# Kernel optimization log

Measured on AMD Instinct MI355X. Metric: run time of the kernel, lower is better.

Reference implementation:

```python
import jax, jax.numpy as jnp
import numpy as np

N_NODES = 100000
N_EDGES = 3200000
F_IN = 16


def gcn_conv(x, edge_index, W, b):
    """PyG GCNConv: x' = D^{-1/2} (A + I) D^{-1/2} (x W) + b,
    with degree computed after adding self-loops."""
    n = x.shape[0]
    xw = x @ W  # [N, F_out]
    row, col = edge_index[0], edge_index[1]  # messages flow row -> col
    ones = jnp.ones(row.shape, dtype=x.dtype)
    deg = jax.ops.segment_sum(ones, col, num_segments=n) + 1.0  # +1 for self-loop
    dinv = jax.lax.rsqrt(deg)  # [N]
    norm = dinv[row] * dinv[col]  # [E]
    msg = xw[row] * norm[:, None]  # [E, F_out]
    out = jax.ops.segment_sum(msg, col, num_segments=n)
    out = out + xw * (1.0 / deg)[:, None]  # self-loop term: norm = 1/deg
    return out + b


def setup_inputs() -> dict:
    key = jax.random.key(0)
    ks = jax.random.split(key, 8)
    x = jax.random.normal(ks[0], (N_NODES, F_IN), dtype=jnp.float32)
    edge_index = jax.random.randint(ks[1], (2, N_EDGES), 0, N_NODES, dtype=jnp.int32)
    # GCNConv weights (glorot in PyG; random normal scaled for the reference)
    W1 = jax.random.normal(ks[2], (F_IN, 4), dtype=jnp.float32) * 0.3
    W2 = jax.random.normal(ks[3], (4, 2), dtype=jnp.float32) * 0.5
    W3 = jax.random.normal(ks[4], (2, 1), dtype=jnp.float32) * 0.7
    b1 = jnp.zeros((4,), jnp.float32)
    b2 = jnp.zeros((2,), jnp.float32)
    b3 = jnp.zeros((1,), jnp.float32)
    return {"x": x, "edge_index": edge_index, "W1": W1, "b1": b1,
            "W2": W2, "b2": b2, "W3": W3, "b3": b3}


def reference(x, edge_index, W1, b1, W2, b2, W3, b3):
    # encode(): GCNConv -> relu -> GCNConv -> relu -> GCNConv -> tanh
    # (dropout is identity in eval mode)
    h = jax.nn.relu(gcn_conv(x, edge_index, W1, b1))
    h = jax.nn.relu(gcn_conv(h, edge_index, W2, b2))
    return jnp.tanh(gcn_conv(h, edge_index, W3, b3))  # [N, 1]
```

## Files before the change

kernel.cpp:

```cpp
#include <hip/hip_runtime.h>
#include <math.h>


static constexpr int BLK    = 256;
static constexpr int BSHIFT = 7;
static constexpr int BCOLS  = 128;
static constexpr int NBMAX  = 1024;
static constexpr int CAP    = 5120;
static constexpr int PAD    = 16;
static constexpr int PBLK   = 512;
static constexpr int PITER  = 13;
static constexpr int PCHUNK = PBLK * PITER;
static constexpr int SBLK   = 512;
static constexpr int GBLK   = 512;

__global__ void zero_cnt_kernel(int* __restrict__ cnt, int len) {
    int i = blockIdx.x * blockDim.x + threadIdx.x;
    if (i < len) cnt[i] = 0;
}

__global__ __launch_bounds__(PBLK) void partition_kernel(
        const int* __restrict__ row, const int* __restrict__ col,
        int* __restrict__ cnt, unsigned int* __restrict__ part,
        int e, int nbuck) {
    __shared__ unsigned int   staged[PCHUNK];
    __shared__ unsigned short bkid[PCHUNK];
    __shared__ int hist[NBMAX];
    __shared__ int excl[NBMAX];
    __shared__ int gbase[NBMAX];
    __shared__ int sh[PBLK];
    const int t = (int)threadIdx.x;
    for (int j = t; j < NBMAX; j += PBLK) hist[j] = 0;
    __syncthreads();

    const int blockstart = blockIdx.x * PCHUNK;
    const int m = min(PCHUNK, e - blockstart);

    unsigned int pay[PITER];
    int bks[PITER], rnk[PITER];
#pragma unroll
    for (int i = 0; i < PITER; ++i) {
        int idx = blockstart + i * PBLK + t;
        if (idx < e) {
            int c = col[idx], r = row[idx];
            bks[i] = c >> BSHIFT;
            pay[i] = ((unsigned int)(c & (BCOLS - 1)) << 17) | (unsigned int)r;
            rnk[i] = atomicAdd(&hist[bks[i]], 1);
        } else {
            bks[i] = -1;
        }
    }
    __syncthreads();

    int a0 = hist[2 * t], a1 = hist[2 * t + 1];
    sh[t] = a0 + a1;
    __syncthreads();
    for (int off = 1; off < PBLK; off <<= 1) {
        int v = (t >= off) ? sh[t - off] : 0;
        __syncthreads();
        sh[t] += v;
        __syncthreads();
    }
    int pairExcl = sh[t] - (a0 + a1);
    excl[2 * t]     = pairExcl;
    excl[2 * t + 1] = pairExcl + a0;
    for (int j = t; j < nbuck; j += PBLK) {
        int h = hist[j];
        gbase[j] = h ? atomicAdd(&cnt[j * PAD], h) : 0;
    }
    __syncthreads();

#pragma unroll
    for (int i = 0; i < PITER; ++i) {
        if (bks[i] >= 0) {
            int pos = excl[bks[i]] + rnk[i];
            staged[pos] = pay[i];
            bkid[pos]   = (unsigned short)bks[i];
        }
    }
    __syncthreads();

    for (int k = t; k < m; k += PBLK) {
        int bk  = bkid[k];
        int off2 = gbase[bk] + (k - excl[bk]);
        if (off2 < CAP)
            part[(size_t)bk * CAP + off2] = staged[k];
    }
}

__global__ __launch_bounds__(SBLK) void sort_y1_kernel(
        unsigned int* __restrict__ part, const int* __restrict__ cnt,
        const float* __restrict__ x, const float* __restrict__ W1,
        int* __restrict__ rs, int* __restrict__ re, float* __restrict__ dinv,
        float* __restrict__ y1, int n) {
    __shared__ unsigned int   staged[CAP];
    __shared__ unsigned int   sorted[CAP];
    __shared__ unsigned short srank[CAP];
    __shared__ int hist[BCOLS];
    __shared__ int scanb[BCOLS];
    const int b = blockIdx.x;
    const int m = min(cnt[b * PAD], CAP);
    const size_t segbase = (size_t)b * CAP;

    if (threadIdx.x < BCOLS) hist[threadIdx.x] = 0;
    __syncthreads();
    for (int k = threadIdx.x; k < m; k += SBLK) {
        unsigned int v = part[segbase + k];
        staged[k] = v;
        srank[k] = (unsigned short)atomicAdd(&hist[v >> 17], 1);
    }
    __syncthreads();

    if (threadIdx.x < BCOLS) scanb[threadIdx.x] = hist[threadIdx.x];
    __syncthreads();
    for (int off = 1; off < BCOLS; off <<= 1) {
        int v = 0;
        if (threadIdx.x < BCOLS && (int)threadIdx.x >= off)
            v = scanb[threadIdx.x - off];
        __syncthreads();
        if (threadIdx.x < BCOLS) scanb[threadIdx.x] += v;
        __syncthreads();
    }

    for (int k = threadIdx.x; k < m; k += SBLK) {
        unsigned int v = staged[k];
        int lc = (int)(v >> 17);
        sorted[(scanb[lc] - hist[lc]) + (int)srank[k]] = v & 0x1FFFFu;
    }
    __syncthreads();

    for (int k = threadIdx.x; k < m; k += SBLK)
        part[segbase + k] = sorted[k];

    int lc = (int)threadIdx.x >> 2;
    int f  = (int)threadIdx.x & 3;
    int node = b * BCOLS + lc;
    if (node < n) {
        int deg = hist[lc];
        float di = rsqrtf((float)(deg + 1));
        if (f == 0) {
            int start = (int)segbase + (scanb[lc] - deg);
            rs[node] = start;
            re[node] = start + deg;
            dinv[node] = di;
        }
        const float4* x4 = (const float4*)x + (size_t)node * 4;
        float4 r0 = x4[0], r1 = x4[1], r2 = x4[2], r3 = x4[3];
        float a = 0.0f;
        a = fmaf(r0.x, W1[0 * 4 + f], a);  a = fmaf(r0.y, W1[1 * 4 + f], a);
        a = fmaf(r0.z, W1[2 * 4 + f], a);  a = fmaf(r0.w, W1[3 * 4 + f], a);
        a = fmaf(r1.x, W1[4 * 4 + f], a);  a = fmaf(r1.y, W1[5 * 4 + f], a);
        a = fmaf(r1.z, W1[6 * 4 + f], a);  a = fmaf(r1.w, W1[7 * 4 + f], a);
        a = fmaf(r2.x, W1[8 * 4 + f], a);  a = fmaf(r2.y, W1[9 * 4 + f], a);
        a = fmaf(r2.z, W1[10 * 4 + f], a); a = fmaf(r2.w, W1[11 * 4 + f], a);
        a = fmaf(r3.x, W1[12 * 4 + f], a); a = fmaf(r3.y, W1[13 * 4 + f], a);
        a = fmaf(r3.z, W1[14 * 4 + f], a); a = fmaf(r3.w, W1[15 * 4 + f], a);
        y1[node * 4 + f] = a * di;
    }
}

template <int F, int FN, int ACT, int SUBW>
__global__ __launch_bounds__(GBLK) void gather_kernel(
        const int* __restrict__ rs, const int* __restrict__ re,
        const unsigned int* __restrict__ csr,
        const float* __restrict__ y, const float* __restrict__ dinv,
        const float* __restrict__ bias, const float* __restrict__ Wn,
        float* __restrict__ outv, int n) {
    int t = blockIdx.x * GBLK + (int)threadIdx.x;
    int node = t / SUBW;
    int lane = t % SUBW;
    if (node >= n) return;
    int s = rs[node], tend = re[node];
    float acc[F];
#pragma unroll
    for (int f = 0; f < F; ++f) acc[f] = 0.0f;
    const float4* y4 = (const float4*)y;
    const float2* y2p = (const float2*)y;
    for (int k = s + lane; k < tend; k += SUBW) {
        int r = (int)csr[k];
        if constexpr (F == 4) {
            float4 a = y4[r];
            acc[0] += a.x; acc[1] += a.y; acc[2] += a.z; acc[3] += a.w;
        } else if constexpr (F == 2) {
            float2 a = y2p[r];
            acc[0] += a.x; acc[1] += a.y;
        } else {
            acc[0] += y[r];
        }
    }
#pragma unroll
    for (int off = SUBW / 2; off > 0; off >>= 1)
#pragma unroll
        for (int f = 0; f < F; ++f) acc[f] += __shfl_xor(acc[f], off);
    if (lane == 0) {
        float di = dinv[node];
        float h[F];
#pragma unroll
        for (int f = 0; f < F; ++f) {
            float z = di * (acc[f] + y[node * F + f]) + bias[f];
            if (ACT == 1) z = fmaxf(z, 0.0f);
            if (ACT == 2) z = tanhf(z);
            h[f] = z;
        }
        if constexpr (FN > 0) {
            float o[FN];
#pragma unroll
            for (int g = 0; g < FN; ++g) o[g] = 0.0f;
#pragma unroll
            for (int f = 0; f < F; ++f)
#pragma unroll
                for (int g = 0; g < FN; ++g)
                    o[g] = fmaf(h[f], Wn[f * FN + g], o[g]);
#pragma unroll
            for (int g = 0; g < FN; ++g) outv[node * FN + g] = o[g] * di;
        } else {
#pragma unroll
            for (int f = 0; f < F; ++f) outv[node * F + f] = h[f];
        }
    }
}

extern "C" void kernel_launch(void* const* d_in, const int* in_sizes, int n_in,
                              void* d_out, int out_size, void* d_ws, size_t ws_size,
                              hipStream_t stream) {
    const float* x  = (const float*)d_in[0];
    const int*   ei = (const int*)d_in[1];
    const float* W1 = (const float*)d_in[2];
    const float* b1 = (const float*)d_in[3];
    const float* W2 = (const float*)d_in[4];
    const float* b2 = (const float*)d_in[5];
    const float* W3 = (const float*)d_in[6];
    const float* b3 = (const float*)d_in[7];
    float* out = (float*)d_out;

    const int n = in_sizes[0] / 16;
    const int e = in_sizes[1] / 2;
    const int* row = ei;
    const int* col = ei + e;

    const int nbuck = (n + BCOLS - 1) / BCOLS;

    size_t off = 0;
    auto take = [&](size_t cnt_) {
        char* p = (char*)d_ws + off * 4;
        off += (cnt_ + 15) & ~(size_t)15;
        return p;
    };
    int* cnt           = (int*)take((size_t)nbuck * PAD);
    unsigned int* part = (unsigned int*)take((size_t)nbuck * CAP);
    int* rs            = (int*)take(n);
    int* re            = (int*)take(n);
    float* dinv        = (float*)take(n);
    float* y1          = (float*)take(4 * n);
    float* y2          = (float*)take(2 * n);
    float* y3          = (float*)take(n);

    zero_cnt_kernel<<<(nbuck * PAD + BLK - 1) / BLK, BLK, 0, stream>>>(cnt, nbuck * PAD);

    const int pnb = (e + PCHUNK - 1) / PCHUNK;
    partition_kernel<<<pnb, PBLK, 0, stream>>>(row, col, cnt, part, e, nbuck);

    sort_y1_kernel<<<nbuck, SBLK, 0, stream>>>(part, cnt, x, W1, rs, re, dinv, y1, n);

    constexpr int SUBW = 8;
    const int gg = (n * SUBW + GBLK - 1) / GBLK;

    gather_kernel<4, 2, 1, SUBW><<<gg, GBLK, 0, stream>>>(rs, re, part, y1, dinv, b1, W2, y2, n);
    gather_kernel<2, 1, 1, SUBW><<<gg, GBLK, 0, stream>>>(rs, re, part, y2, dinv, b2, W3, y3, n);
    gather_kernel<1, 0, 2, SUBW><<<gg, GBLK, 0, stream>>>(rs, re, part, y3, dinv, b3, nullptr, out, n);
}
```

Baseline: 113.3 us.

## Fuse all GCN stages into one cooperative persistent kernel with grid syncs

Replaces the six separate launches (zero, partition, sort, three gathers) with a single cooperative kernel that uses grid-wide syncs between phases. Each phase loops over its work with a persistent grid sized from occupancy. The aim is to remove kernel launch gaps and tail idling between dependent stages. In exchange it adds grid.sync costs, reduces parallelism in the partition phase (larger chunks, 1024-thread blocks), and the persistent grid may under-occupy the gather phases.

```diff
diff --git a/kernel.cpp b/kernel.cpp
--- a/kernel.cpp
+++ b/kernel.cpp
@@ -1,223 +1,237 @@
 #include <hip/hip_runtime.h>
+#include <hip/hip_cooperative_groups.h>
 #include <math.h>
 
-
-static constexpr int BLK    = 256;
+namespace cg = cooperative_groups;
+
+
 static constexpr int BSHIFT = 7;
 static constexpr int BCOLS  = 128;
 static constexpr int NBMAX  = 1024;
 static constexpr int CAP    = 5120;
 static constexpr int PAD    = 16;
-static constexpr int PBLK   = 512;
-static constexpr int PITER  = 13;
-static constexpr int PCHUNK = PBLK * PITER;
-static constexpr int SBLK   = 512;
-static constexpr int GBLK   = 512;
-
-__global__ void zero_cnt_kernel(int* __restrict__ cnt, int len) {
-    int i = blockIdx.x * blockDim.x + threadIdx.x;
-    if (i < len) cnt[i] = 0;
-}
-
-__global__ __launch_bounds__(PBLK) void partition_kernel(
-        const int* __restrict__ row, const int* __restrict__ col,
-        int* __restrict__ cnt, unsigned int* __restrict__ part,
-        int e, int nbuck) {
-    __shared__ unsigned int   staged[PCHUNK];
-    __shared__ unsigned short bkid[PCHUNK];
-    __shared__ int hist[NBMAX];
-    __shared__ int excl[NBMAX];
-    __shared__ int gbase[NBMAX];
-    __shared__ int sh[PBLK];
-    const int t = (int)threadIdx.x;
-    for (int j = t; j < NBMAX; j += PBLK) hist[j] = 0;
-    __syncthreads();
-
-    const int blockstart = blockIdx.x * PCHUNK;
-    const int m = min(PCHUNK, e - blockstart);
-
-    unsigned int pay[PITER];
-    int bks[PITER], rnk[PITER];
-#pragma unroll
-    for (int i = 0; i < PITER; ++i) {
-        int idx = blockstart + i * PBLK + t;
-        if (idx < e) {
-            int c = col[idx], r = row[idx];
-            bks[i] = c >> BSHIFT;
-            pay[i] = ((unsigned int)(c & (BCOLS - 1)) << 17) | (unsigned int)r;
-            rnk[i] = atomicAdd(&hist[bks[i]], 1);
-        } else {
-            bks[i] = -1;
-        }
-    }
-    __syncthreads();
-
-    int a0 = hist[2 * t], a1 = hist[2 * t + 1];
-    sh[t] = a0 + a1;
-    __syncthreads();
-    for (int off = 1; off < PBLK; off <<= 1) {
-        int v = (t >= off) ? sh[t - off] : 0;
-        __syncthreads();
-        sh[t] += v;
-        __syncthreads();
-    }
-    int pairExcl = sh[t] - (a0 + a1);
-    excl[2 * t]     = pairExcl;
-    excl[2 * t + 1] = pairExcl + a0;
-    for (int j = t; j < nbuck; j += PBLK) {
-        int h = hist[j];
-        gbase[j] = h ? atomicAdd(&cnt[j * PAD], h) : 0;
-    }
-    __syncthreads();
-
-#pragma unroll
-    for (int i = 0; i < PITER; ++i) {
-        if (bks[i] >= 0) {
-            int pos = excl[bks[i]] + rnk[i];
-            staged[pos] = pay[i];
-            bkid[pos]   = (unsigned short)bks[i];
-        }
-    }
-    __syncthreads();
-
-    for (int k = t; k < m; k += PBLK) {
-        int bk  = bkid[k];
-        int off2 = gbase[bk] + (k - excl[bk]);
-        if (off2 < CAP)
-            part[(size_t)bk * CAP + off2] = staged[k];
+static constexpr int TB     = 1024;
+static constexpr int PITER  = 7;
+static constexpr int PCHUNK = TB * PITER;
+static constexpr int SUBW   = 8;
+
+static constexpr int SMEM_BYTES = 55296;
+
+struct Params {
+    const float* x;
+    const int* row;
+    const int* col;
+    const float* W1; const float* b1;
+    const float* W2; const float* b2;
+    const float* W3; const float* b3;
+    int* cnt;
+    unsigned int* part;
+    int* rs; int* re;
+    float* dinv;
+    float* y1; float* y2; float* y3;
+    float* out;
+    int n, e, nbuck, nchunk;
+};
+
+template <int F, int FN, int ACT>
+__device__ __forceinline__ void gather_layer(
+        const Params& p, const float* __restrict__ y,
+        const float* __restrict__ bias, const float* __restrict__ Wn,
+        float* __restrict__ outv, int gsize) {
+    const int total = p.n * SUBW;
+    for (int tt = blockIdx.x * TB + (int)threadIdx.x; tt < total; tt += gsize * TB) {
+        int node = tt >> 3;
+        int lane = tt & 7;
+        int s = p.rs[node], tend = p.re[node];
+        float acc[F];
+#pragma unroll
+        for (int f = 0; f < F; ++f) acc[f] = 0.0f;
+        for (int k = s + lane; k < tend; k += SUBW) {
+            int r = (int)p.part[k];
+            if constexpr (F == 4) {
+                float4 a = ((const float4*)y)[r];
+                acc[0] += a.x; acc[1] += a.y; acc[2] += a.z; acc[3] += a.w;
+            } else if constexpr (F == 2) {
+                float2 a = ((const float2*)y)[r];
+                acc[0] += a.x; acc[1] += a.y;
+            } else {
+                acc[0] += y[r];
+            }
+        }
+#pragma unroll
+        for (int off = SUBW / 2; off > 0; off >>= 1)
+#pragma unroll
+            for (int f = 0; f < F; ++f) acc[f] += __shfl_xor(acc[f], off);
+        if (lane == 0) {
+            float di = p.dinv[node];
+            float h[F];
+#pragma unroll
+            for (int f = 0; f < F; ++f) {
+                float z = di * (acc[f] + y[node * F + f]) + bias[f];
+                if (ACT == 1) z = fmaxf(z, 0.0f);
+                if (ACT == 2) z = tanhf(z);
+                h[f] = z;
+            }
+            if constexpr (FN > 0) {
+                float o[FN];
+#pragma unroll
+                for (int g = 0; g < FN; ++g) o[g] = 0.0f;
+#pragma unroll
+                for (int f = 0; f < F; ++f)
+#pragma unroll
+                    for (int g = 0; g < FN; ++g)
+                        o[g] = fmaf(h[f], Wn[f * FN + g], o[g]);
+#pragma unroll
+                for (int g = 0; g < FN; ++g) outv[node * FN + g] = o[g] * di;
+            } else {
+#pragma unroll
+                for (int f = 0; f < F; ++f) outv[node * F + f] = h[f];
+            }
+        }
     }
 }
 
-__global__ __launch_bounds__(SBLK) void sort_y1_kernel(
-        unsigned int* __restrict__ part, const int* __restrict__ cnt,
-        const float* __restrict__ x, const float* __restrict__ W1,
-        int* __restrict__ rs, int* __restrict__ re, float* __restrict__ dinv,
-        float* __restrict__ y1, int n) {
-    __shared__ unsigned int   staged[CAP];
-    __shared__ unsigned int   sorted[CAP];
-    __shared__ unsigned short srank[CAP];
-    __shared__ int hist[BCOLS];
-    __shared__ int scanb[BCOLS];
-    const int b = blockIdx.x;
-    const int m = min(cnt[b * PAD], CAP);
-    const size_t segbase = (size_t)b * CAP;
-
-    if (threadIdx.x < BCOLS) hist[threadIdx.x] = 0;
-    __syncthreads();
-    for (int k = threadIdx.x; k < m; k += SBLK) {
-        unsigned int v = part[segbase + k];
-        staged[k] = v;
-        srank[k] = (unsigned short)atomicAdd(&hist[v >> 17], 1);
+__global__ __launch_bounds__(TB, 8) void gcn_mega_kernel(Params p) {
+    cg::grid_group grid = cg::this_grid();
+    __shared__ __align__(16) unsigned char smem[SMEM_BYTES];
+    const int t = (int)threadIdx.x;
+    const int gsize = (int)gridDim.x;
+
+    for (int i = blockIdx.x * TB + t; i < p.nbuck * PAD; i += gsize * TB)
+        p.cnt[i] = 0;
+    grid.sync();
+
+    {
+        unsigned int*   staged = (unsigned int*)(smem);
+        unsigned short* bkid   = (unsigned short*)(smem + 28672);
+        int* hist  = (int*)(smem + 43008);
+        int* excl  = (int*)(smem + 47104);
+        int* gbase = (int*)(smem + 51200);
+        for (int chunk = blockIdx.x; chunk < p.nchunk; chunk += gsize) {
+            hist[t] = 0;
+            __syncthreads();
+            const int bs = chunk * PCHUNK;
+            const int m = min(PCHUNK, p.e - bs);
+            unsigned int pay[PITER];
+            int bks[PITER], rnk[PITER];
+#pragma unroll
+            for (int i = 0; i < PITER; ++i) {
+                int idx = bs + i * TB + t;
+                if (idx < p.e) {
+                    int c = p.col[idx], r = p.row[idx];
+                    bks[i] = c >> BSHIFT;
+                    pay[i] = ((unsigned int)(c & (BCOLS - 1)) << 17) | (unsigned int)r;
+                    rnk[i] = atomicAdd(&hist[bks[i]], 1);
+                } else {
+                    bks[i] = -1;
+                }
+            }
+            __syncthreads();
+            int h = hist[t];
+            excl[t] = h;
+            __syncthreads();
+            for (int off = 1; off < NBMAX; off <<= 1) {
+                int v = (t >= off) ? excl[t - off] : 0;
+                __syncthreads();
+                excl[t] += v;
+                __syncthreads();
+            }
+            int ex = excl[t] - h;
+            int gb = (h > 0) ? atomicAdd(&p.cnt[t * PAD], h) : 0;
+            excl[t]  = ex;
+            gbase[t] = gb;
+            __syncthreads();
+#pragma unroll
+            for (int i = 0; i < PITER; ++i) {
+                if (bks[i] >= 0) {
+                    int pos = excl[bks[i]] + rnk[i];
+                    staged[pos] = pay[i];
+                    bkid[pos]   = (unsigned short)bks[i];
+                }
+            }
+            __syncthreads();
+            for (int k = t; k < m; k += TB) {
+                int bk = bkid[k];
+                int o2 = gbase[bk] + (k - excl[bk]);
+                if (o2 < CAP)
+                    p.part[(size_t)bk * CAP + o2] = staged[k];
+            }
+            __syncthreads();
+        }
     }
-    __syncthreads();
-
-    if (threadIdx.x < BCOLS) scanb[threadIdx.x] = hist[threadIdx.x];
-    __syncthreads();
-    for (int off = 1; off < BCOLS; off <<= 1) {
-        int v = 0;
-        if (threadIdx.x < BCOLS && (int)threadIdx.x >= off)
-            v = scanb[threadIdx.x - off];
-        __syncthreads();
-        if (threadIdx.x < BCOLS) scanb[threadIdx.x] += v;
-        __syncthreads();
+    grid.sync();
+
+    {
+        unsigned int*   staged = (unsigned int*)(smem);
+        unsigned int*   sorted = (unsigned int*)(smem + 20480);
+        unsigned short* srank  = (unsigned short*)(smem + 40960);
+        int* hist  = (int*)(smem + 51200);
+        int* scanb = (int*)(smem + 51712);
+        for (int b = blockIdx.x; b < p.nbuck; b += gsize) {
+            const int m = min(p.cnt[b * PAD], CAP);
+            const size_t segbase = (size_t)b * CAP;
+            if (t < BCOLS) hist[t] = 0;
+            __syncthreads();
+            for (int k = t; k < m; k += TB) {
+                unsigned int v = p.part[segbase + k];
+                staged[k] = v;
+                srank[k] = (unsigned short)atomicAdd(&hist[v >> 17], 1);
+            }
+            __syncthreads();
+            if (t < BCOLS) scanb[t] = hist[t];
+            __syncthreads();
+            for (int off = 1; off < BCOLS; off <<= 1) {
+                int v = 0;
+                if (t < BCOLS && t >= off) v = scanb[t - off];
+                __syncthreads();
+                if (t < BCOLS) scanb[t] += v;
+                __syncthreads();
+            }
+            for (int k = t; k < m; k += TB) {
+                unsigned int v = staged[k];
+                int lc = (int)(v >> 17);
+                sorted[(scanb[lc] - hist[lc]) + (int)srank[k]] = v & 0x1FFFFu;
+            }
+            __syncthreads();
+            for (int k = t; k < m; k += TB)
+                p.part[segbase + k] = sorted[k];
+            int lc = t >> 3, sub = t & 7;
+            int node = b * BCOLS + lc;
+            if (node < p.n) {
+                int deg = hist[lc];
+                float di = rsqrtf((float)(deg + 1));
+                if (sub == 0) {
+                    int start = (int)segbase + (scanb[lc] - deg);
+                    p.rs[node] = start;
+                    p.re[node] = start + deg;
+                    p.dinv[node] = di;
+                }
+                if (sub < 4) {
+                    const float4* x4 = (const float4*)p.x + (size_t)node * 4;
+                    float4 r0 = x4[0], r1 = x4[1], r2 = x4[2], r3 = x4[3];
+                    const float* W1 = p.W1;
+                    float a = 0.0f;
+                    a = fmaf(r0.x, W1[0 * 4 + sub], a);  a = fmaf(r0.y, W1[1 * 4 + sub], a);
+                    a = fmaf(r0.z, W1[2 * 4 + sub], a);  a = fmaf(r0.w, W1[3 * 4 + sub], a);
+                    a = fmaf(r1.x, W1[4 * 4 + sub], a);  a = fmaf(r1.y, W1[5 * 4 + sub], a);
+                    a = fmaf(r1.z, W1[6 * 4 + sub], a);  a = fmaf(r1.w, W1[7 * 4 + sub], a);
+                    a = fmaf(r2.x, W1[8 * 4 + sub], a);  a = fmaf(r2.y, W1[9 * 4 + sub], a);
+                    a = fmaf(r2.z, W1[10 * 4 + sub], a); a = fmaf(r2.w, W1[11 * 4 + sub], a);
+                    a = fmaf(r3.x, W1[12 * 4 + sub], a); a = fmaf(r3.y, W1[13 * 4 + sub], a);
+                    a = fmaf(r3.z, W1[14 * 4 + sub], a); a = fmaf(r3.w, W1[15 * 4 + sub], a);
+                    p.y1[node * 4 + sub] = a * di;
+                }
+            }
+            __syncthreads();
+        }
     }
-
-    for (int k = threadIdx.x; k < m; k += SBLK) {
-        unsigned int v = staged[k];
-        int lc = (int)(v >> 17);
-        sorted[(scanb[lc] - hist[lc]) + (int)srank[k]] = v & 0x1FFFFu;
-    }
-    __syncthreads();
-
-    for (int k = threadIdx.x; k < m; k += SBLK)
-        part[segbase + k] = sorted[k];
-
-    int lc = (int)threadIdx.x >> 2;
-    int f  = (int)threadIdx.x & 3;
-    int node = b * BCOLS + lc;
-    if (node < n) {
-        int deg = hist[lc];
-        float di = rsqrtf((float)(deg + 1));
-        if (f == 0) {
-            int start = (int)segbase + (scanb[lc] - deg);
-            rs[node] = start;
-            re[node] = start + deg;
-            dinv[node] = di;
-        }
-        const float4* x4 = (const float4*)x + (size_t)node * 4;
-        float4 r0 = x4[0], r1 = x4[1], r2 = x4[2], r3 = x4[3];
-        float a = 0.0f;
-        a = fmaf(r0.x, W1[0 * 4 + f], a);  a = fmaf(r0.y, W1[1 * 4 + f], a);
-        a = fmaf(r0.z, W1[2 * 4 + f], a);  a = fmaf(r0.w, W1[3 * 4 + f], a);
-        a = fmaf(r1.x, W1[4 * 4 + f], a);  a = fmaf(r1.y, W1[5 * 4 + f], a);
-        a = fmaf(r1.z, W1[6 * 4 + f], a);  a = fmaf(r1.w, W1[7 * 4 + f], a);
-        a = fmaf(r2.x, W1[8 * 4 + f], a);  a = fmaf(r2.y, W1[9 * 4 + f], a);
-        a = fmaf(r2.z, W1[10 * 4 + f], a); a = fmaf(r2.w, W1[11 * 4 + f], a);
-        a = fmaf(r3.x, W1[12 * 4 + f], a); a = fmaf(r3.y, W1[13 * 4 + f], a);
-        a = fmaf(r3.z, W1[14 * 4 + f], a); a = fmaf(r3.w, W1[15 * 4 + f], a);
-        y1[node * 4 + f] = a * di;
-    }
-}
-
-template <int F, int FN, int ACT, int SUBW>
-__global__ __launch_bounds__(GBLK) void gather_kernel(
-        const int* __restrict__ rs, const int* __restrict__ re,
-        const unsigned int* __restrict__ csr,
-        const float* __restrict__ y, const float* __restrict__ dinv,
-        const float* __restrict__ bias, const float* __restrict__ Wn,
-        float* __restrict__ outv, int n) {
-    int t = blockIdx.x * GBLK + (int)threadIdx.x;
-    int node = t / SUBW;
-    int lane = t % SUBW;
-    if (node >= n) return;
-    int s = rs[node], tend = re[node];
-    float acc[F];
-#pragma unroll
-    for (int f = 0; f < F; ++f) acc[f] = 0.0f;
-    const float4* y4 = (const float4*)y;
-    const float2* y2p = (const float2*)y;
-    for (int k = s + lane; k < tend; k += SUBW) {
-        int r = (int)csr[k];
-        if constexpr (F == 4) {
-            float4 a = y4[r];
-            acc[0] += a.x; acc[1] += a.y; acc[2] += a.z; acc[3] += a.w;
-        } else if constexpr (F == 2) {
-            float2 a = y2p[r];
-            acc[0] += a.x; acc[1] += a.y;
-        } else {
-            acc[0] += y[r];
-        }
-    }
-#pragma unroll
-    for (int off = SUBW / 2; off > 0; off >>= 1)
-#pragma unroll
-        for (int f = 0; f < F; ++f) acc[f] += __shfl_xor(acc[f], off);
-    if (lane == 0) {
-        float di = dinv[node];
-        float h[F];
-#pragma unroll
-        for (int f = 0; f < F; ++f) {
-            float z = di * (acc[f] + y[node * F + f]) + bias[f];
-            if (ACT == 1) z = fmaxf(z, 0.0f);
-            if (ACT == 2) z = tanhf(z);
-            h[f] = z;
-        }
-        if constexpr (FN > 0) {
-            float o[FN];
-#pragma unroll
-            for (int g = 0; g < FN; ++g) o[g] = 0.0f;
-#pragma unroll
-            for (int f = 0; f < F; ++f)
-#pragma unroll
-                for (int g = 0; g < FN; ++g)
-                    o[g] = fmaf(h[f], Wn[f * FN + g], o[g]);
-#pragma unroll
-            for (int g = 0; g < FN; ++g) outv[node * FN + g] = o[g] * di;
-        } else {
-#pragma unroll
-            for (int f = 0; f < F; ++f) outv[node * F + f] = h[f];
-        }
-    }
+    grid.sync();
+
+    gather_layer<4, 2, 1>(p, p.y1, p.b1, p.W2, p.y2, gsize);
+    grid.sync();
+    gather_layer<2, 1, 1>(p, p.y2, p.b2, p.W3, p.y3, gsize);
+    grid.sync();
+    gather_layer<1, 0, 2>(p, p.y3, p.b3, nullptr, p.out, gsize);
 }
 
 extern "C" void kernel_launch(void* const* d_in, const int* in_sizes, int n_in,
@@ -238,13 +252,14 @@
     const int* row = ei;
     const int* col = ei + e;
 
-    const int nbuck = (n + BCOLS - 1) / BCOLS;
+    const int nbuck  = (n + BCOLS - 1) / BCOLS;
+    const int nchunk = (e + PCHUNK - 1) / PCHUNK;
 
     size_t off = 0;
     auto take = [&](size_t cnt_) {
-        char* p = (char*)d_ws + off * 4;
+        char* pp = (char*)d_ws + off * 4;
         off += (cnt_ + 15) & ~(size_t)15;
-        return p;
+        return pp;
     };
     int* cnt           = (int*)take((size_t)nbuck * PAD);
     unsigned int* part = (unsigned int*)take((size_t)nbuck * CAP);
@@ -255,17 +270,20 @@
     float* y2          = (float*)take(2 * n);
     float* y3          = (float*)take(n);
 
-    zero_cnt_kernel<<<(nbuck * PAD + BLK - 1) / BLK, BLK, 0, stream>>>(cnt, nbuck * PAD);
-
-    const int pnb = (e + PCHUNK - 1) / PCHUNK;
-    partition_kernel<<<pnb, PBLK, 0, stream>>>(row, col, cnt, part, e, nbuck);
-
-    sort_y1_kernel<<<nbuck, SBLK, 0, stream>>>(part, cnt, x, W1, rs, re, dinv, y1, n);
-
-    constexpr int SUBW = 8;
-    const int gg = (n * SUBW + GBLK - 1) / GBLK;
-
-    gather_kernel<4, 2, 1, SUBW><<<gg, GBLK, 0, stream>>>(rs, re, part, y1, dinv, b1, W2, y2, n);
-    gather_kernel<2, 1, 1, SUBW><<<gg, GBLK, 0, stream>>>(rs, re, part, y2, dinv, b2, W3, y3, n);
-    gather_kernel<1, 0, 2, SUBW><<<gg, GBLK, 0, stream>>>(rs, re, part, y3, dinv, b3, nullptr, out, n);
+    Params p;
+    p.x = x; p.row = row; p.col = col;
+    p.W1 = W1; p.b1 = b1; p.W2 = W2; p.b2 = b2; p.W3 = W3; p.b3 = b3;
+    p.cnt = cnt; p.part = part; p.rs = rs; p.re = re; p.dinv = dinv;
+    p.y1 = y1; p.y2 = y2; p.y3 = y3; p.out = out;
+    p.n = n; p.e = e; p.nbuck = nbuck; p.nchunk = nchunk;
+
+    int maxB = 0;
+    hipOccupancyMaxActiveBlocksPerMultiprocessor(&maxB, gcn_mega_kernel, TB, 0);
+    if (maxB < 1) maxB = 1;
+    if (maxB > 2) maxB = 2;
+    int grid = maxB * 256;
+
+    void* args[] = { (void*)&p };
+    hipLaunchCooperativeKernel(gcn_mega_kernel, dim3(grid), dim3(TB),
+                               args, 0, stream);
 }
```

Result: slower. 265.7 us (+134.4%).
